# Optimization experiments

Hardware: AMD Instinct MI355X
Metric: run time of the kernel (lower is better)

Reference implementation:

```python
import jax, jax.numpy as jnp
import numpy as np

BN_EPS = 1e-3


def _bn(x, gamma, beta):
    # training-mode BatchNorm1d: per-call batch statistics (biased variance)
    m = jnp.mean(x, axis=0)
    v = jnp.mean(jnp.square(x - m), axis=0)
    return gamma * (x - m) * jax.lax.rsqrt(v + BN_EPS) + beta


def setup_inputs() -> dict:
    key = jax.random.key(0)
    ks = jax.random.split(key, 8)
    N, V, Cin, Cout = 1_000_000, 100_000, 16, 64
    return {
        "feat": jax.random.normal(ks[0], (V, Cin), dtype=jnp.float32),
        "points_xyz": jax.random.normal(ks[1], (N, Cin), dtype=jnp.float32),
        "unq_inv": jax.random.randint(ks[2], (N,), 0, V),
        "W_pre": jax.random.normal(ks[3], (Cin, Cout), dtype=jnp.float32) * (1.0 / np.sqrt(Cin)),
        "b_pre": jnp.zeros((Cout,), dtype=jnp.float32),
        "gamma_pre": jnp.ones((Cout,), dtype=jnp.float32),
        "beta_pre": jnp.zeros((Cout,), dtype=jnp.float32),
        "W_pos": jax.random.normal(ks[4], (Cout, Cout), dtype=jnp.float32) * (1.0 / np.sqrt(Cout)),
        "b_pos": jnp.zeros((Cout,), dtype=jnp.float32),
        "gamma_n": jnp.ones((Cout,), dtype=jnp.float32),
        "beta_n": jnp.zeros((Cout,), dtype=jnp.float32),
    }


def reference(feat, points_xyz, unq_inv, W_pre, b_pre, gamma_pre, beta_pre,
              W_pos, b_pos, gamma_n, beta_n):
    V = feat.shape[0]
    # per-point branch: pre_mix (Linear + BN), sin/cos gating, scatter-add to voxels
    p = _bn(points_xyz @ W_pre + b_pre, gamma_pre, beta_pre)      # [N, Cout]
    pw = p @ W_pos + b_pos                                        # [N, Cout]
    feat_add_sin = jax.ops.segment_sum(p * jnp.sin(pw), unq_inv, num_segments=V)  # [V, Cout]
    feat_add_cos = jax.ops.segment_sum(p * jnp.cos(pw), unq_inv, num_segments=V)
    # per-voxel (center) branch through the SAME pre_mix / pos_weight layers
    f = _bn(feat @ W_pre + b_pre, gamma_pre, beta_pre)            # [V, Cout]
    mw = f @ W_pos + b_pos
    center_sin = f * jnp.sin(mw)
    center_cos = f * jnp.cos(mw)
    final = (feat_add_sin + center_sin) * center_sin + (feat_add_cos + center_cos) * center_cos
    return jax.nn.relu(_bn(final, gamma_n, beta_n))
```

## Files before the change

kernel.cpp:

```cpp
#include <hip/hip_runtime.h>
#include <cstdint>
#include <cstddef>

constexpr int CIN  = 16;
constexpr int COUT = 64;
constexpr int NMOM = 16 + 136;
constexpr double BN_EPS = 1e-3;

typedef float v2f __attribute__((ext_vector_type(2)));
constexpr float INV_2PI = 0.15915494309189535f;

constexpr int P_A = 0, P_B = 64, P_C = 128, P_WC = 192, P_SZ = 192 + CIN * COUT;

constexpr int CHUNK = 512;
constexpr int MB = 256;

__global__ __launch_bounds__(256) void moments2_kernel(const float* __restrict__ xyz, int n1,
                                                       const float* __restrict__ feat, int n2,
                                                       const int* __restrict__ unq,
                                                       int* __restrict__ cnt,
                                                       float* __restrict__ partP,
                                                       float* __restrict__ partF)
{
    const int bb  = blockIdx.x;
    const bool second = (bb >= MB);
    const float* x = second ? feat : xyz;
    const int    n = second ? n2 : n1;
    float* part    = second ? partF : partP;
    const int blk  = second ? bb - MB : bb;

    float acc[NMOM];
#pragma unroll
    for (int i = 0; i < NMOM; i++) acc[i] = 0.f;

    int tid = blk * 256 + threadIdx.x;
    int stride = MB * 256;
    for (int r = tid; r < n; r += stride) {
        const float4* xp = (const float4*)(x + (size_t)r * CIN);
        float4 a0 = xp[0], a1 = xp[1], a2 = xp[2], a3 = xp[3];
        if (!second) atomicAdd(cnt + unq[r], 1);
        float v[16] = {a0.x,a0.y,a0.z,a0.w, a1.x,a1.y,a1.z,a1.w,
                       a2.x,a2.y,a2.z,a2.w, a3.x,a3.y,a3.z,a3.w};
#pragma unroll
        for (int i = 0; i < 16; i++) acc[i] += v[i];
        int c = 16;
#pragma unroll
        for (int k = 0; k < 16; k++)
#pragma unroll
            for (int l = k; l < 16; l++) { acc[c] = fmaf(v[k], v[l], acc[c]); c++; }
    }

    const int lane = threadIdx.x & 63;
    const int wid  = threadIdx.x >> 6;
    float r0 = 0.f, r1 = 0.f, r2 = 0.f;
#pragma unroll
    for (int i = 0; i < NMOM; i++) {
        float s = acc[i];
#pragma unroll
        for (int off = 1; off < 64; off <<= 1) s += __shfl_xor(s, off, 64);
        if (i < 64)       { if (lane == i)       r0 = s; }
        else if (i < 128) { if (lane == i - 64)  r1 = s; }
        else              { if (lane == i - 128) r2 = s; }
    }

    __shared__ float red[4][NMOM];
    red[wid][lane] = r0;
    red[wid][64 + lane] = r1;
    if (lane < NMOM - 128) red[wid][128 + lane] = r2;
    __syncthreads();
    int t = threadIdx.x;
    if (t < NMOM) {
        float s = red[0][t] + red[1][t] + red[2][t] + red[3][t];
        part[(size_t)blk * NMOM + t] = s;
    }
}

__global__ __launch_bounds__(256) void prep_kernel(const float* __restrict__ Wpre, const float* __restrict__ bpre,
                            const float* __restrict__ gpre, const float* __restrict__ bepre,
                            const float* __restrict__ Wpos, const float* __restrict__ bpos,
                            const float* __restrict__ partP, const float* __restrict__ partF,
                            int nrows, int Np, int Vv,
                            float* __restrict__ prepP, float* __restrict__ prepF)
{
    const int t  = threadIdx.x;
    const int br = blockIdx.x;
    const float* part = br ? partF : partP;
    const double n    = br ? (double)Vv : (double)Np;
    const double inv_n = 1.0 / n;
    float* prep       = br ? prepF : prepP;

    __shared__ float sWpre[CIN * 64];
    __shared__ float sWpos[64 * 64];
    __shared__ double mom[NMOM];
    __shared__ double sS[64], sB[64];

    for (int i = t; i < CIN * 64; i += 256) sWpre[i] = Wpre[i];
    for (int i = t; i < 64 * 64; i += 256)  sWpos[i] = Wpos[i];

    if (t < NMOM) {
        double s0 = 0, s1 = 0, s2 = 0, s3 = 0, s4 = 0, s5 = 0, s6 = 0, s7 = 0;
        int r = 0;
        for (; r + 8 <= nrows; r += 8) {
            s0 += (double)part[(size_t)(r + 0) * NMOM + t];
            s1 += (double)part[(size_t)(r + 1) * NMOM + t];
            s2 += (double)part[(size_t)(r + 2) * NMOM + t];
            s3 += (double)part[(size_t)(r + 3) * NMOM + t];
            s4 += (double)part[(size_t)(r + 4) * NMOM + t];
            s5 += (double)part[(size_t)(r + 5) * NMOM + t];
            s6 += (double)part[(size_t)(r + 6) * NMOM + t];
            s7 += (double)part[(size_t)(r + 7) * NMOM + t];
        }
        for (; r < nrows; r++) s0 += (double)part[(size_t)r * NMOM + t];
        mom[t] = ((s0 + s1) + (s2 + s3)) + ((s4 + s5) + (s6 + s7));
    }
    __syncthreads();

    if (t < 64) {
        const int k = t;
        double mu[16];
#pragma unroll
        for (int i = 0; i < 16; i++) mu[i] = mom[i] * inv_n;
        double w[16];
#pragma unroll
        for (int i = 0; i < 16; i++) w[i] = (double)sWpre[i * 64 + k];

        double mk = (double)bpre[k];
#pragma unroll
        for (int i = 0; i < 16; i++) mk += mu[i] * w[i];

        double var = 0.0;
        int c = 16;
#pragma unroll
        for (int a = 0; a < 16; a++)
#pragma unroll
            for (int l = a; l < 16; l++) {
                double cov = mom[c] * inv_n - mu[a] * mu[l]; c++;
                var += (a == l ? 1.0 : 2.0) * w[a] * w[l] * cov;
            }

        double s_k = (double)gpre[k] / sqrt(var + BN_EPS);
        double B_k = (double)bepre[k] + s_k * ((double)bpre[k] - mk);
        sS[k] = s_k; sB[k] = B_k;
    }
    __syncthreads();

    if (t < 64) {
        const int k = t;
        double c0 = (double)bpos[k], c1 = 0.0;
        for (int j = 0; j < 64; j += 2) {
            c0 += sB[j]     * (double)sWpos[j * 64 + k];
            c1 += sB[j + 1] * (double)sWpos[(j + 1) * 64 + k];
        }
        prep[P_A + k] = (float)sS[k];
        prep[P_B + k] = (float)sB[k];
        prep[P_C + k] = (float)(c0 + c1);
    }

    {
        const int k  = t & 63;
        const int i0 = t >> 6;
        for (int i = i0; i < 16; i += 4) {
            double w0 = 0.0, w1 = 0.0;
            for (int j = 0; j < 64; j += 2) {
                w0 += (double)sWpre[i * 64 + j]     * sS[j]     * (double)sWpos[j * 64 + k];
                w1 += (double)sWpre[i * 64 + j + 1] * sS[j + 1] * (double)sWpos[(j + 1) * 64 + k];
            }
            prep[P_WC + i * 64 + k] = (float)(w0 + w1);
        }
    }
}

__global__ __launch_bounds__(256) void scan_a(const int* __restrict__ cnt, int V,
                                              int* __restrict__ chunkSum)
{
    const int b = blockIdx.x, t = threadIdx.x;
    int base = b * CHUNK;
    int i0 = base + t * 2, i1 = i0 + 1;
    int s = ((i0 < V) ? cnt[i0] : 0) + ((i1 < V) ? cnt[i1] : 0);
    __shared__ int red[4];
    const int lane = t & 63, wid = t >> 6;
#pragma unroll
    for (int off = 1; off < 64; off <<= 1) s += __shfl_xor(s, off, 64);
    if (lane == 0) red[wid] = s;
    __syncthreads();
    if (t == 0) chunkSum[b] = red[0] + red[1] + red[2] + red[3];
}

__global__ __launch_bounds__(256) void scan_b(const int* __restrict__ chunkSum, int nch,
                                              int* __restrict__ chunkBase,
                                              int* __restrict__ start, int V, int N)
{
    const int t = threadIdx.x;
    __shared__ int a[256];
    int v = (t < nch) ? chunkSum[t] : 0;
    a[t] = v;
    __syncthreads();
    for (int off = 1; off < 256; off <<= 1) {
        int add = (t >= off) ? a[t - off] : 0;
        __syncthreads();
        a[t] += add;
        __syncthreads();
    }
    chunkBase[t] = a[t] - v;
    if (t == 0) start[V] = N;
}

__global__ __launch_bounds__(64) void scan_c(const int* __restrict__ cnt, int V,
                                             const int* __restrict__ chunkBase,
                                             int* __restrict__ start)
{
    const int b = blockIdx.x;
    const int lane = threadIdx.x;
    const int base = b * CHUNK + lane * 8;
    int e[8];
    int run = 0;
#pragma unroll
    for (int j = 0; j < 8; j++) {
        int idx = base + j;
        int c = (idx < V) ? cnt[idx] : 0;
        e[j] = run;
        run += c;
    }
    int incl = run;
#pragma unroll
    for (int off = 1; off < 64; off <<= 1) {
        int vv = __shfl_up(incl, off, 64);
        if (lane >= off) incl += vv;
    }
    int excl = incl - run;
    int myBase = chunkBase[b] + excl;
#pragma unroll
    for (int j = 0; j < 8; j++) {
        int idx = base + j;
        if (idx < V) start[idx] = myBase + e[j];
    }
}

__global__ __launch_bounds__(256) void scatter_kernel(const int* __restrict__ unq, int N,
                                                      const int* __restrict__ start,
                                                      int* __restrict__ cursor,
                                                      int* __restrict__ sortedIdx)
{
    int t = blockIdx.x * blockDim.x + threadIdx.x;
    int stride = gridDim.x * blockDim.x;
    for (; t < N; t += stride) {
        int v = unq[t];
        int pos = start[v] + atomicAdd(cursor + v, 1);
        sortedIdx[pos] = t;
    }
}

__global__ __launch_bounds__(256) void fused_pass(const float* __restrict__ xyz,
                                                  const float* __restrict__ feat,
                                                  const int* __restrict__ sortedIdx,
                                                  const int* __restrict__ start,
                                                  const float* __restrict__ Wpre,
                                                  const float* __restrict__ prepP,
                                                  const float* __restrict__ prepF,
                                                  float* __restrict__ outFinal,
                                                  float* __restrict__ statsPart, int V)
{
    const int lane = threadIdx.x & 63;
    const int wid  = threadIdx.x >> 6;
    const int rq   = lane >> 2;
    const int cc   = lane & 3;

    __shared__ float4 ldsq[4][3][64];
    __shared__ float  sWcF[CIN * 64];
    float4* bufA = ldsq[wid][0];
    float4* bufB = ldsq[wid][1];
    float4* remb = ldsq[wid][2];
    const int wslot = rq * 4 + cc;

    for (int i = threadIdx.x; i < CIN * 64; i += 256) sWcF[i] = prepF[P_WC + i];
    __syncthreads();

    v2f wP[16];
#pragma unroll
    for (int i = 0; i < 16; i++)
        wP[i] = (v2f){Wpre[i * 64 + lane], prepP[P_WC + i * 64 + lane]};

    const float AP = prepP[P_A + lane], BP = prepP[P_B + lane];
    const float CPr = prepP[P_C + lane] * INV_2PI;
    const float AF = prepF[P_A + lane], BF = prepF[P_B + lane];
    const float CFr = prepF[P_C + lane] * INV_2PI;

    const int wave = __builtin_amdgcn_readfirstlane((int)((blockIdx.x * blockDim.x + threadIdx.x) >> 6));
    const int nw   = (gridDim.x * blockDim.x) >> 6;
    float s1 = 0.f, s2 = 0.f;

    auto prefetch = [&](int v, int& sb, int& m, float4& q) {
        sb = __builtin_amdgcn_readfirstlane(start[v]);
        int se = __builtin_amdgcn_readfirstlane(start[v + 1]);
        m = se - sb;
        int ms0 = min(m, 15);
        int row = min(rq, ms0);
        int ridx = sortedIdx[sb + row];
        const float* bp = (row == ms0) ? (feat + (size_t)v * CIN)
                                       : (xyz  + (size_t)ridx * CIN);
        q = *(const float4*)(bp + cc * 4);
    };

    auto pointrow = [&](const float4* buf, int j, v2f& acc) {
        float4 c0 = buf[j * 4 + 0], c1 = buf[j * 4 + 1],
               c2 = buf[j * 4 + 2], c3 = buf[j * 4 + 3];
        float xs[16] = {c0.x,c0.y,c0.z,c0.w, c1.x,c1.y,c1.z,c1.w,
                        c2.x,c2.y,c2.z,c2.w, c3.x,c3.y,c3.z,c3.w};
        v2f d = (v2f){0.f, 0.f};
#pragma unroll
        for (int i = 0; i < 16; i++) d += xs[i] * wP[i];
        float p  = fmaf(AP, d.x, BP);
        float r  = fmaf(d.y, INV_2PI, CPr);
        float sv = __builtin_amdgcn_sinf(r);
        float cv = __builtin_amdgcn_cosf(r);
        acc += p * (v2f){sv, cv};
    };

    int v = wave;
    int sb = 0, m = 0;
    float4* cur = bufA;
    float4* nxt = bufB;
    if (v < V) {
        float4 q; prefetch(v, sb, m, q);
        cur[wslot] = q;
    }

    while (v < V) {
        const int vn = v + nw;
        int sbn = 0, mn = 0; float4 qn = {};
        if (vn < V) prefetch(vn, sbn, mn, qn);

        const int ms0 = min(m, 15);
        v2f acc = (v2f){0.f, 0.f};

        for (int j = 0; j < ms0; j++) pointrow(cur, j, acc);

        for (int base = 15; base < m; base += 16) {
            const int msr  = min(16, m - base);
            const int rowc = min(rq, msr - 1);
            int ridx = sortedIdx[sb + base + rowc];
            remb[wslot] = *(const float4*)(xyz + (size_t)ridx * CIN + cc * 4);
            for (int j = 0; j < msr; j++) pointrow(remb, j, acc);
        }

        {
            float4 c0 = cur[ms0 * 4 + 0], c1 = cur[ms0 * 4 + 1],
                   c2 = cur[ms0 * 4 + 2], c3 = cur[ms0 * 4 + 3];
            float xs[16] = {c0.x,c0.y,c0.z,c0.w, c1.x,c1.y,c1.z,c1.w,
                            c2.x,c2.y,c2.z,c2.w, c3.x,c3.y,c3.z,c3.w};
            float dx = 0.f, dw = 0.f;
#pragma unroll
            for (int i = 0; i < 16; i++) {
                dx = fmaf(xs[i], wP[i].x, dx);
                dw = fmaf(xs[i], sWcF[i * 64 + lane], dw);
            }
            float f  = fmaf(AF, dx, BF);
            float r  = fmaf(dw, INV_2PI, CFr);
            float sv = __builtin_amdgcn_sinf(r);
            float cv = __builtin_amdgcn_cosf(r);
            float cs = f * sv, ccn = f * cv;
            float fin = fmaf(acc.x + cs, cs, (acc.y + ccn) * ccn);
            outFinal[(size_t)v * 64 + lane] = fin;
            s1 += fin;
            s2 = fmaf(fin, fin, s2);
        }

        if (vn < V) nxt[wslot] = qn;
        float4* tmp = cur; cur = nxt; nxt = tmp;
        v = vn; sb = sbn; m = mn;
    }

    __shared__ float sh1[4][64], sh2[4][64];
    sh1[wid][lane] = s1; sh2[wid][lane] = s2;
    __syncthreads();
    if (threadIdx.x < 64) {
        float t1 = sh1[0][lane] + sh1[1][lane] + sh1[2][lane] + sh1[3][lane];
        float t2 = sh2[0][lane] + sh2[1][lane] + sh2[2][lane] + sh2[3][lane];
        float* row = statsPart + (size_t)(blockIdx.x & 63) * 128;
        atomicAdd(row + lane, t1);
        atomicAdd(row + 64 + lane, t2);
    }
}

__global__ __launch_bounds__(256) void norm_kernel(float* __restrict__ out,
                                                   const float* __restrict__ sp,
                                                   const float* __restrict__ gn,
                                                   const float* __restrict__ bnb,
                                                   int V, size_t n4)
{
    __shared__ float sNs[64], sNb[64];
    const int t = threadIdx.x;
    if (t < 64) {
        double u1 = 0.0, u2 = 0.0;
#pragma unroll 4
        for (int r = 0; r < 64; r++) {
            u1 += (double)sp[(size_t)r * 128 + t];
            u2 += (double)sp[(size_t)r * 128 + 64 + t];
        }
        double mean = u1 / (double)V;
        double var  = u2 / (double)V - mean * mean;
        double ns   = (double)gn[t] / sqrt(var + BN_EPS);
        sNs[t] = (float)ns;
        sNb[t] = (float)((double)bnb[t] - ns * mean);
    }
    __syncthreads();

    const float4* ns4 = (const float4*)sNs;
    const float4* nb4 = (const float4*)sNb;
    float4* o4 = (float4*)out;
    size_t i = (size_t)blockIdx.x * blockDim.x + threadIdx.x;
    size_t stride = (size_t)gridDim.x * blockDim.x;
    for (; i < n4; i += stride) {
        int g = (int)(i & 15);
        float4 sc = ns4[g], bi = nb4[g];
        float4 w = o4[i];
        w.x = fmaxf(0.f, fmaf(sc.x, w.x, bi.x));
        w.y = fmaxf(0.f, fmaf(sc.y, w.y, bi.y));
        w.z = fmaxf(0.f, fmaf(sc.z, w.z, bi.z));
        w.w = fmaxf(0.f, fmaf(sc.w, w.w, bi.w));
        o4[i] = w;
    }
}

extern "C" void kernel_launch(void* const* d_in, const int* in_sizes, int n_in,
                              void* d_out, int out_size, void* d_ws, size_t ws_size,
                              hipStream_t stream)
{
    const float* feat  = (const float*)d_in[0];
    const float* xyz   = (const float*)d_in[1];
    const int*   unq   = (const int*)d_in[2];
    const float* Wpre  = (const float*)d_in[3];
    const float* bpre  = (const float*)d_in[4];
    const float* gpre  = (const float*)d_in[5];
    const float* bepre = (const float*)d_in[6];
    const float* Wpos  = (const float*)d_in[7];
    const float* bpos  = (const float*)d_in[8];
    const float* gn    = (const float*)d_in[9];
    const float* bnb   = (const float*)d_in[10];

    const int V = in_sizes[0] / CIN;
    const int N = in_sizes[1] / CIN;
    const int nch = (V + CHUNK - 1) / CHUNK;

    char* ws = (char*)d_ws;
    size_t off = 0;
    auto alloc = [&](size_t bytes) { void* p = ws + off; off += (bytes + 255) & ~size_t(255); return p; };

    int*   cnt       = (int*)alloc((size_t)V * 4);
    int*   cursor    = (int*)alloc((size_t)V * 4);
    float* statsPart = (float*)alloc(64 * 128 * 4);
    const size_t zeroBytes = off;

    int*   start     = (int*)alloc((size_t)(V + 1) * 4);
    int*   chunkSum  = (int*)alloc(256 * 4);
    int*   chunkBase = (int*)alloc(256 * 4);
    int*   sortedIdx = (int*)alloc((size_t)(N + 64) * 4);

    float* partP = (float*)alloc((size_t)MB * NMOM * 4);
    float* partF = (float*)alloc((size_t)MB * NMOM * 4);
    float* prepP = (float*)alloc(P_SZ * 4);
    float* prepF = (float*)alloc(P_SZ * 4);

    hipMemsetAsync(d_ws, 0, zeroBytes, stream);

    moments2_kernel<<<2 * MB, 256, 0, stream>>>(xyz, N, feat, V, unq, cnt, partP, partF);
    scan_a<<<nch, 256, 0, stream>>>(cnt, V, chunkSum);
    scan_b<<<1, 256, 0, stream>>>(chunkSum, nch, chunkBase, start, V, N);
    scan_c<<<nch, 64, 0, stream>>>(cnt, V, chunkBase, start);
    scatter_kernel<<<1024, 256, 0, stream>>>(unq, N, start, cursor, sortedIdx);
    prep_kernel<<<2, 256, 0, stream>>>(Wpre, bpre, gpre, bepre, Wpos, bpos,
                                       partP, partF, MB, N, V, prepP, prepF);
    fused_pass<<<2048, 256, 0, stream>>>(xyz, feat, sortedIdx, start, Wpre,
                                         prepP, prepF, (float*)d_out, statsPart, V);
    norm_kernel<<<512, 256, 0, stream>>>((float*)d_out, statsPart, gn, bnb, V,
                                         (size_t)out_size / 4);
}
```

Measured before the change: 233.8 us.

## Merge prep with scan chunk sums, fold scan_b into scanC, software-pipeline LDS row loads

```diff
diff --git a/kernel.cpp b/kernel.cpp
--- a/kernel.cpp
+++ b/kernel.cpp
@@ -75,14 +75,32 @@
     }
 }
 
-__global__ __launch_bounds__(256) void prep_kernel(const float* __restrict__ Wpre, const float* __restrict__ bpre,
+__global__ __launch_bounds__(256) void prep_scanA(const float* __restrict__ Wpre, const float* __restrict__ bpre,
                             const float* __restrict__ gpre, const float* __restrict__ bepre,
                             const float* __restrict__ Wpos, const float* __restrict__ bpos,
                             const float* __restrict__ partP, const float* __restrict__ partF,
                             int nrows, int Np, int Vv,
-                            float* __restrict__ prepP, float* __restrict__ prepF)
-{
-    const int t  = threadIdx.x;
+                            float* __restrict__ prepP, float* __restrict__ prepF,
+                            const int* __restrict__ cnt, int V,
+                            int* __restrict__ chunkSum)
+{
+    const int t = threadIdx.x;
+    const int lane = t & 63, wid = t >> 6;
+
+    if (blockIdx.x >= 2) {
+        const int b = blockIdx.x - 2;
+        int base = b * CHUNK;
+        int i0 = base + t * 2, i1 = i0 + 1;
+        int s = ((i0 < V) ? cnt[i0] : 0) + ((i1 < V) ? cnt[i1] : 0);
+        __shared__ int redc[4];
+#pragma unroll
+        for (int off = 1; off < 64; off <<= 1) s += __shfl_xor(s, off, 64);
+        if (lane == 0) redc[wid] = s;
+        __syncthreads();
+        if (t == 0) chunkSum[b] = redc[0] + redc[1] + redc[2] + redc[3];
+        return;
+    }
+
     const int br = blockIdx.x;
     const float* part = br ? partF : partP;
     const double n    = br ? (double)Vv : (double)Np;
@@ -170,47 +188,20 @@
     }
 }
 
-__global__ __launch_bounds__(256) void scan_a(const int* __restrict__ cnt, int V,
-                                              int* __restrict__ chunkSum)
-{
-    const int b = blockIdx.x, t = threadIdx.x;
-    int base = b * CHUNK;
-    int i0 = base + t * 2, i1 = i0 + 1;
-    int s = ((i0 < V) ? cnt[i0] : 0) + ((i1 < V) ? cnt[i1] : 0);
-    __shared__ int red[4];
-    const int lane = t & 63, wid = t >> 6;
-#pragma unroll
-    for (int off = 1; off < 64; off <<= 1) s += __shfl_xor(s, off, 64);
-    if (lane == 0) red[wid] = s;
-    __syncthreads();
-    if (t == 0) chunkSum[b] = red[0] + red[1] + red[2] + red[3];
-}
-
-__global__ __launch_bounds__(256) void scan_b(const int* __restrict__ chunkSum, int nch,
-                                              int* __restrict__ chunkBase,
-                                              int* __restrict__ start, int V, int N)
-{
-    const int t = threadIdx.x;
-    __shared__ int a[256];
-    int v = (t < nch) ? chunkSum[t] : 0;
-    a[t] = v;
-    __syncthreads();
-    for (int off = 1; off < 256; off <<= 1) {
-        int add = (t >= off) ? a[t - off] : 0;
-        __syncthreads();
-        a[t] += add;
-        __syncthreads();
-    }
-    chunkBase[t] = a[t] - v;
-    if (t == 0) start[V] = N;
-}
-
-__global__ __launch_bounds__(64) void scan_c(const int* __restrict__ cnt, int V,
-                                             const int* __restrict__ chunkBase,
-                                             int* __restrict__ start)
+__global__ __launch_bounds__(64) void scanC(const int* __restrict__ cnt, int V, int N,
+                                            const int* __restrict__ chunkSum,
+                                            int* __restrict__ start,
+                                            int* __restrict__ cursor)
 {
     const int b = blockIdx.x;
     const int lane = threadIdx.x;
+
+    int pv = 0;
+    for (int i = lane; i < b; i += 64) pv += chunkSum[i];
+#pragma unroll
+    for (int off = 1; off < 64; off <<= 1) pv += __shfl_xor(pv, off, 64);
+    const int chunkBase = pv;
+
     const int base = b * CHUNK + lane * 8;
     int e[8];
     int run = 0;
@@ -228,12 +219,13 @@
         if (lane >= off) incl += vv;
     }
     int excl = incl - run;
-    int myBase = chunkBase[b] + excl;
+    int myBase = chunkBase + excl;
 #pragma unroll
     for (int j = 0; j < 8; j++) {
         int idx = base + j;
-        if (idx < V) start[idx] = myBase + e[j];
-    }
+        if (idx < V) { start[idx] = myBase + e[j]; cursor[idx] = 0; }
+    }
+    if (b == 0 && lane == 0) start[V] = N;
 }
 
 __global__ __launch_bounds__(256) void scatter_kernel(const int* __restrict__ unq, int N,
@@ -301,9 +293,7 @@
         q = *(const float4*)(bp + cc * 4);
     };
 
-    auto pointrow = [&](const float4* buf, int j, v2f& acc) {
-        float4 c0 = buf[j * 4 + 0], c1 = buf[j * 4 + 1],
-               c2 = buf[j * 4 + 2], c3 = buf[j * 4 + 3];
+    auto pointmath = [&](float4 c0, float4 c1, float4 c2, float4 c3, v2f& acc) {
         float xs[16] = {c0.x,c0.y,c0.z,c0.w, c1.x,c1.y,c1.z,c1.w,
                         c2.x,c2.y,c2.z,c2.w, c3.x,c3.y,c3.z,c3.w};
         v2f d = (v2f){0.f, 0.f};
@@ -333,14 +323,24 @@
         const int ms0 = min(m, 15);
         v2f acc = (v2f){0.f, 0.f};
 
-        for (int j = 0; j < ms0; j++) pointrow(cur, j, acc);
+        if (ms0 > 0) {
+            float4 r0 = cur[0], r1 = cur[1], r2 = cur[2], r3 = cur[3];
+            for (int j = 0; j + 1 < ms0; j++) {
+                float4 n0 = cur[(j+1)*4+0], n1 = cur[(j+1)*4+1],
+                       n2 = cur[(j+1)*4+2], n3 = cur[(j+1)*4+3];
+                pointmath(r0, r1, r2, r3, acc);
+                r0 = n0; r1 = n1; r2 = n2; r3 = n3;
+            }
+            pointmath(r0, r1, r2, r3, acc);
+        }
 
         for (int base = 15; base < m; base += 16) {
             const int msr  = min(16, m - base);
             const int rowc = min(rq, msr - 1);
             int ridx = sortedIdx[sb + base + rowc];
             remb[wslot] = *(const float4*)(xyz + (size_t)ridx * CIN + cc * 4);
-            for (int j = 0; j < msr; j++) pointrow(remb, j, acc);
+            for (int j = 0; j < msr; j++)
+                pointmath(remb[j*4+0], remb[j*4+1], remb[j*4+2], remb[j*4+3], acc);
         }
 
         {
@@ -447,13 +447,12 @@
     auto alloc = [&](size_t bytes) { void* p = ws + off; off += (bytes + 255) & ~size_t(255); return p; };
 
     int*   cnt       = (int*)alloc((size_t)V * 4);
-    int*   cursor    = (int*)alloc((size_t)V * 4);
     float* statsPart = (float*)alloc(64 * 128 * 4);
     const size_t zeroBytes = off;
 
+    int*   cursor    = (int*)alloc((size_t)V * 4);
     int*   start     = (int*)alloc((size_t)(V + 1) * 4);
     int*   chunkSum  = (int*)alloc(256 * 4);
-    int*   chunkBase = (int*)alloc(256 * 4);
     int*   sortedIdx = (int*)alloc((size_t)(N + 64) * 4);
 
     float* partP = (float*)alloc((size_t)MB * NMOM * 4);
@@ -464,12 +463,11 @@
     hipMemsetAsync(d_ws, 0, zeroBytes, stream);
 
     moments2_kernel<<<2 * MB, 256, 0, stream>>>(xyz, N, feat, V, unq, cnt, partP, partF);
-    scan_a<<<nch, 256, 0, stream>>>(cnt, V, chunkSum);
-    scan_b<<<1, 256, 0, stream>>>(chunkSum, nch, chunkBase, start, V, N);
-    scan_c<<<nch, 64, 0, stream>>>(cnt, V, chunkBase, start);
+    prep_scanA<<<nch + 2, 256, 0, stream>>>(Wpre, bpre, gpre, bepre, Wpos, bpos,
+                                            partP, partF, MB, N, V, prepP, prepF,
+                                            cnt, V, chunkSum);
+    scanC<<<nch, 64, 0, stream>>>(cnt, V, N, chunkSum, start, cursor);
     scatter_kernel<<<1024, 256, 0, stream>>>(unq, N, start, cursor, sortedIdx);
-    prep_kernel<<<2, 256, 0, stream>>>(Wpre, bpre, gpre, bepre, Wpos, bpos,
-                                       partP, partF, MB, N, V, prepP, prepF);
     fused_pass<<<2048, 256, 0, stream>>>(xyz, feat, sortedIdx, start, Wpre,
                                          prepP, prepF, (float*)d_out, statsPart, V);
     norm_kernel<<<512, 256, 0, stream>>>((float*)d_out, statsPart, gn, bnb, V,
```

After: 244.8 us. 1.05x slower.

## Add per-voxel 16-slot index table and deepen prefetch pipeline to two voxels

Applied to the files above, without the earlier changes.

```diff
diff --git a/kernel.cpp b/kernel.cpp
--- a/kernel.cpp
+++ b/kernel.cpp
@@ -239,37 +239,41 @@
 __global__ __launch_bounds__(256) void scatter_kernel(const int* __restrict__ unq, int N,
                                                       const int* __restrict__ start,
                                                       int* __restrict__ cursor,
-                                                      int* __restrict__ sortedIdx)
+                                                      int* __restrict__ sortedIdx,
+                                                      int* __restrict__ table16)
 {
     int t = blockIdx.x * blockDim.x + threadIdx.x;
     int stride = gridDim.x * blockDim.x;
     for (; t < N; t += stride) {
         int v = unq[t];
-        int pos = start[v] + atomicAdd(cursor + v, 1);
-        sortedIdx[pos] = t;
+        int slot = atomicAdd(cursor + v, 1);
+        sortedIdx[start[v] + slot] = t;
+        if (slot < 15) table16[v * 16 + slot] = t;
     }
 }
 
 __global__ __launch_bounds__(256) void fused_pass(const float* __restrict__ xyz,
                                                   const float* __restrict__ feat,
+                                                  const int* __restrict__ table16,
+                                                  const int* __restrict__ cnt,
                                                   const int* __restrict__ sortedIdx,
                                                   const int* __restrict__ start,
                                                   const float* __restrict__ Wpre,
                                                   const float* __restrict__ prepP,
                                                   const float* __restrict__ prepF,
                                                   float* __restrict__ outFinal,
-                                                  float* __restrict__ statsPart, int V)
+                                                  float* __restrict__ statsPart,
+                                                  int V, int N)
 {
     const int lane = threadIdx.x & 63;
     const int wid  = threadIdx.x >> 6;
     const int rq   = lane >> 2;
     const int cc   = lane & 3;
 
-    __shared__ float4 ldsq[4][3][64];
+    __shared__ float4 ldsq[4][2][64];
     __shared__ float  sWcF[CIN * 64];
-    float4* bufA = ldsq[wid][0];
-    float4* bufB = ldsq[wid][1];
-    float4* remb = ldsq[wid][2];
+    float4* cur = ldsq[wid][0];
+    float4* nxt = ldsq[wid][1];
     const int wslot = rq * 4 + cc;
 
     for (int i = threadIdx.x; i < CIN * 64; i += 256) sWcF[i] = prepF[P_WC + i];
@@ -289,19 +293,20 @@
     const int nw   = (gridDim.x * blockDim.x) >> 6;
     float s1 = 0.f, s2 = 0.f;
 
-    auto prefetch = [&](int v, int& sb, int& m, float4& q) {
-        sb = __builtin_amdgcn_readfirstlane(start[v]);
-        int se = __builtin_amdgcn_readfirstlane(start[v + 1]);
-        m = se - sb;
-        int ms0 = min(m, 15);
-        int row = min(rq, ms0);
-        int ridx = sortedIdx[sb + row];
-        const float* bp = (row == ms0) ? (feat + (size_t)v * CIN)
-                                       : (xyz  + (size_t)ridx * CIN);
+    auto issueIdx = [&](int v, int& cReg, int& tReg) {
+        cReg = cnt[v];
+        tReg = table16[v * 16 + rq];
+    };
+    auto gatherRow = [&](int v, int tIdx, float4& q) {
+        const float* bp;
+        if (rq == 15) bp = feat + (size_t)v * CIN;
+        else {
+            int ridx = min(max(tIdx, 0), N - 1);
+            bp = xyz + (size_t)ridx * CIN;
+        }
         q = *(const float4*)(bp + cc * 4);
     };
-
-    auto pointrow = [&](const float4* buf, int j, v2f& acc) {
+    auto pointmath = [&](const float4* buf, int j, v2f& acc) {
         float4 c0 = buf[j * 4 + 0], c1 = buf[j * 4 + 1],
                c2 = buf[j * 4 + 2], c3 = buf[j * 4 + 3];
         float xs[16] = {c0.x,c0.y,c0.z,c0.w, c1.x,c1.y,c1.z,c1.w,
@@ -316,36 +321,44 @@
         acc += p * (v2f){sv, cv};
     };
 
-    int v = wave;
-    int sb = 0, m = 0;
-    float4* cur = bufA;
-    float4* nxt = bufB;
-    if (v < V) {
-        float4 q; prefetch(v, sb, m, q);
+    int v0 = wave, v1 = v0 + nw, v2 = v1 + nw;
+    int m0 = 0, m1 = 0, c2r = 0, t2r = 0;
+    float4 q1 = {};
+
+    if (v0 < V) {
+        int c, t; issueIdx(v0, c, t);
+        m0 = __builtin_amdgcn_readfirstlane(c);
+        float4 q; gatherRow(v0, t, q);
         cur[wslot] = q;
     }
-
-    while (v < V) {
-        const int vn = v + nw;
-        int sbn = 0, mn = 0; float4 qn = {};
-        if (vn < V) prefetch(vn, sbn, mn, qn);
-
-        const int ms0 = min(m, 15);
+    if (v1 < V) {
+        int c, t; issueIdx(v1, c, t);
+        m1 = __builtin_amdgcn_readfirstlane(c);
+        gatherRow(v1, t, q1);
+    }
+    if (v2 < V) issueIdx(v2, c2r, t2r);
+
+    while (v0 < V) {
+        const int ms0 = min(m0, 15);
         v2f acc = (v2f){0.f, 0.f};
 
-        for (int j = 0; j < ms0; j++) pointrow(cur, j, acc);
-
-        for (int base = 15; base < m; base += 16) {
-            const int msr  = min(16, m - base);
-            const int rowc = min(rq, msr - 1);
-            int ridx = sortedIdx[sb + base + rowc];
-            remb[wslot] = *(const float4*)(xyz + (size_t)ridx * CIN + cc * 4);
-            for (int j = 0; j < msr; j++) pointrow(remb, j, acc);
+        for (int j = 0; j < ms0; j++) pointmath(cur, j, acc);
+
+        if (m0 > 15) {
+            const int sb = __builtin_amdgcn_readfirstlane(start[v0]);
+            for (int base = 15; base < m0; base += 16) {
+                const int msr  = min(16, m0 - base);
+                const int rowc = min(rq, msr - 1);
+                int ridx = sortedIdx[sb + base + rowc];
+                nxt[wslot] = *(const float4*)(xyz + (size_t)ridx * CIN + cc * 4);
+                for (int j = 0; j < msr; j++)
+                    pointmath(nxt, j, acc);
+            }
         }
 
         {
-            float4 c0 = cur[ms0 * 4 + 0], c1 = cur[ms0 * 4 + 1],
-                   c2 = cur[ms0 * 4 + 2], c3 = cur[ms0 * 4 + 3];
+            float4 c0 = cur[15 * 4 + 0], c1 = cur[15 * 4 + 1],
+                   c2 = cur[15 * 4 + 2], c3 = cur[15 * 4 + 3];
             float xs[16] = {c0.x,c0.y,c0.z,c0.w, c1.x,c1.y,c1.z,c1.w,
                             c2.x,c2.y,c2.z,c2.w, c3.x,c3.y,c3.z,c3.w};
             float dx = 0.f, dw = 0.f;
@@ -360,14 +373,23 @@
             float cv = __builtin_amdgcn_cosf(r);
             float cs = f * sv, ccn = f * cv;
             float fin = fmaf(acc.x + cs, cs, (acc.y + ccn) * ccn);
-            outFinal[(size_t)v * 64 + lane] = fin;
+            outFinal[(size_t)v0 * 64 + lane] = fin;
             s1 += fin;
             s2 = fmaf(fin, fin, s2);
         }
 
-        if (vn < V) nxt[wslot] = qn;
+        if (v1 < V) nxt[wslot] = q1;
+        int mNew = 0; float4 qNew = {};
+        if (v2 < V) {
+            mNew = __builtin_amdgcn_readfirstlane(c2r);
+            gatherRow(v2, t2r, qNew);
+        }
+        const int v3 = v2 + nw;
+        if (v3 < V) issueIdx(v3, c2r, t2r);
+
         float4* tmp = cur; cur = nxt; nxt = tmp;
-        v = vn; sb = sbn; m = mn;
+        v0 = v1; v1 = v2; v2 = v3;
+        m0 = m1; m1 = mNew; q1 = qNew;
     }
 
     __shared__ float sh1[4][64], sh2[4][64];
@@ -455,6 +477,7 @@
     int*   chunkSum  = (int*)alloc(256 * 4);
     int*   chunkBase = (int*)alloc(256 * 4);
     int*   sortedIdx = (int*)alloc((size_t)(N + 64) * 4);
+    int*   table16   = (int*)alloc((size_t)V * 16 * 4);
 
     float* partP = (float*)alloc((size_t)MB * NMOM * 4);
     float* partF = (float*)alloc((size_t)MB * NMOM * 4);
@@ -467,11 +490,11 @@
     scan_a<<<nch, 256, 0, stream>>>(cnt, V, chunkSum);
     scan_b<<<1, 256, 0, stream>>>(chunkSum, nch, chunkBase, start, V, N);
     scan_c<<<nch, 64, 0, stream>>>(cnt, V, chunkBase, start);
-    scatter_kernel<<<1024, 256, 0, stream>>>(unq, N, start, cursor, sortedIdx);
+    scatter_kernel<<<1024, 256, 0, stream>>>(unq, N, start, cursor, sortedIdx, table16);
     prep_kernel<<<2, 256, 0, stream>>>(Wpre, bpre, gpre, bepre, Wpos, bpos,
                                        partP, partF, MB, N, V, prepP, prepF);
-    fused_pass<<<2048, 256, 0, stream>>>(xyz, feat, sortedIdx, start, Wpre,
-                                         prepP, prepF, (float*)d_out, statsPart, V);
+    fused_pass<<<2048, 256, 0, stream>>>(xyz, feat, table16, cnt, sortedIdx, start,
+                                         Wpre, prepP, prepF, (float*)d_out, statsPart, V, N);
     norm_kernel<<<512, 256, 0, stream>>>((float*)d_out, statsPart, gn, bnb, V,
                                          (size_t)out_size / 4);
 }
```

Measured after the change: 257.0 us. 1.1x slower.

## Use packed fp16 dot products for per-point projections in fused pass

Applied to the files above, without the earlier changes.

```diff
diff --git a/kernel.cpp b/kernel.cpp
--- a/kernel.cpp
+++ b/kernel.cpp
@@ -8,12 +8,16 @@
 constexpr double BN_EPS = 1e-3;
 
 typedef float v2f __attribute__((ext_vector_type(2)));
+typedef __fp16 v2h __attribute__((ext_vector_type(2)));
 constexpr float INV_2PI = 0.15915494309189535f;
 
 constexpr int P_A = 0, P_B = 64, P_C = 128, P_WC = 192, P_SZ = 192 + CIN * COUT;
 
 constexpr int CHUNK = 512;
-constexpr int MB = 256;
+constexpr int MB = 512;
+
+__device__ __forceinline__ unsigned bc_u(v2h h) { return __builtin_bit_cast(unsigned, h); }
+__device__ __forceinline__ v2h bc_h(unsigned u) { return __builtin_bit_cast(v2h, u); }
 
 __global__ __launch_bounds__(256) void moments2_kernel(const float* __restrict__ xyz, int n1,
                                                        const float* __restrict__ feat, int n2,
@@ -265,20 +269,28 @@
     const int rq   = lane >> 2;
     const int cc   = lane & 3;
 
-    __shared__ float4 ldsq[4][3][64];
-    __shared__ float  sWcF[CIN * 64];
-    float4* bufA = ldsq[wid][0];
-    float4* bufB = ldsq[wid][1];
-    float4* remb = ldsq[wid][2];
+    __shared__ uint2 ldsq[4][3][64];
+    __shared__ unsigned sWcF2[8 * 64];
+    uint2* bufA = ldsq[wid][0];
+    uint2* bufB = ldsq[wid][1];
+    uint2* remb = ldsq[wid][2];
     const int wslot = rq * 4 + cc;
 
-    for (int i = threadIdx.x; i < CIN * 64; i += 256) sWcF[i] = prepF[P_WC + i];
-    __syncthreads();
-
-    v2f wP[16];
-#pragma unroll
-    for (int i = 0; i < 16; i++)
-        wP[i] = (v2f){Wpre[i * 64 + lane], prepP[P_WC + i * 64 + lane]};
+    for (int i = threadIdx.x; i < 8 * 64; i += 256) {
+        int fi = i >> 6, ch = i & 63;
+        sWcF2[i] = bc_u(__builtin_amdgcn_cvt_pkrtz(prepF[P_WC + (2 * fi) * 64 + ch],
+                                                   prepF[P_WC + (2 * fi + 1) * 64 + ch]));
+    }
+    __syncthreads();
+
+    v2h wpre2[8], wcp2[8];
+#pragma unroll
+    for (int i = 0; i < 8; i++) {
+        wpre2[i] = __builtin_amdgcn_cvt_pkrtz(Wpre[(2 * i) * 64 + lane],
+                                              Wpre[(2 * i + 1) * 64 + lane]);
+        wcp2[i]  = __builtin_amdgcn_cvt_pkrtz(prepP[P_WC + (2 * i) * 64 + lane],
+                                              prepP[P_WC + (2 * i + 1) * 64 + lane]);
+    }
 
     const float AP = prepP[P_A + lane], BP = prepP[P_B + lane];
     const float CPr = prepP[P_C + lane] * INV_2PI;
@@ -289,7 +301,7 @@
     const int nw   = (gridDim.x * blockDim.x) >> 6;
     float s1 = 0.f, s2 = 0.f;
 
-    auto prefetch = [&](int v, int& sb, int& m, float4& q) {
+    auto prefetch = [&](int v, int& sb, int& m, uint2& u) {
         sb = __builtin_amdgcn_readfirstlane(start[v]);
         int se = __builtin_amdgcn_readfirstlane(start[v + 1]);
         m = se - sb;
@@ -298,19 +310,24 @@
         int ridx = sortedIdx[sb + row];
         const float* bp = (row == ms0) ? (feat + (size_t)v * CIN)
                                        : (xyz  + (size_t)ridx * CIN);
-        q = *(const float4*)(bp + cc * 4);
+        float4 q = *(const float4*)(bp + cc * 4);
+        u.x = bc_u(__builtin_amdgcn_cvt_pkrtz(q.x, q.y));
+        u.y = bc_u(__builtin_amdgcn_cvt_pkrtz(q.z, q.w));
     };
 
-    auto pointrow = [&](const float4* buf, int j, v2f& acc) {
-        float4 c0 = buf[j * 4 + 0], c1 = buf[j * 4 + 1],
-               c2 = buf[j * 4 + 2], c3 = buf[j * 4 + 3];
-        float xs[16] = {c0.x,c0.y,c0.z,c0.w, c1.x,c1.y,c1.z,c1.w,
-                        c2.x,c2.y,c2.z,c2.w, c3.x,c3.y,c3.z,c3.w};
-        v2f d = (v2f){0.f, 0.f};
-#pragma unroll
-        for (int i = 0; i < 16; i++) d += xs[i] * wP[i];
-        float p  = fmaf(AP, d.x, BP);
-        float r  = fmaf(d.y, INV_2PI, CPr);
+    auto pointmath = [&](const uint2* buf, int j, v2f& acc) {
+        uint4 a = ((const uint4*)buf)[j * 2 + 0];
+        uint4 b = ((const uint4*)buf)[j * 2 + 1];
+        v2h xs[8] = {bc_h(a.x), bc_h(a.y), bc_h(a.z), bc_h(a.w),
+                     bc_h(b.x), bc_h(b.y), bc_h(b.z), bc_h(b.w)};
+        float dx = 0.f, dw = 0.f;
+#pragma unroll
+        for (int i = 0; i < 8; i++) {
+            dx = __builtin_amdgcn_fdot2(xs[i], wpre2[i], dx, false);
+            dw = __builtin_amdgcn_fdot2(xs[i], wcp2[i],  dw, false);
+        }
+        float p  = fmaf(AP, dx, BP);
+        float r  = fmaf(dw, INV_2PI, CPr);
         float sv = __builtin_amdgcn_sinf(r);
         float cv = __builtin_amdgcn_cosf(r);
         acc += p * (v2f){sv, cv};
@@ -318,41 +335,45 @@
 
     int v = wave;
     int sb = 0, m = 0;
-    float4* cur = bufA;
-    float4* nxt = bufB;
+    uint2* cur = bufA;
+    uint2* nxt = bufB;
     if (v < V) {
-        float4 q; prefetch(v, sb, m, q);
-        cur[wslot] = q;
+        uint2 u; prefetch(v, sb, m, u);
+        cur[wslot] = u;
     }
 
     while (v < V) {
         const int vn = v + nw;
-        int sbn = 0, mn = 0; float4 qn = {};
-        if (vn < V) prefetch(vn, sbn, mn, qn);
+        int sbn = 0, mn = 0; uint2 un = {};
+        if (vn < V) prefetch(vn, sbn, mn, un);
 
         const int ms0 = min(m, 15);
         v2f acc = (v2f){0.f, 0.f};
 
-        for (int j = 0; j < ms0; j++) pointrow(cur, j, acc);
+        for (int j = 0; j < ms0; j++) pointmath(cur, j, acc);
 
         for (int base = 15; base < m; base += 16) {
             const int msr  = min(16, m - base);
             const int rowc = min(rq, msr - 1);
             int ridx = sortedIdx[sb + base + rowc];
-            remb[wslot] = *(const float4*)(xyz + (size_t)ridx * CIN + cc * 4);
-            for (int j = 0; j < msr; j++) pointrow(remb, j, acc);
+            float4 q = *(const float4*)(xyz + (size_t)ridx * CIN + cc * 4);
+            uint2 u;
+            u.x = bc_u(__builtin_amdgcn_cvt_pkrtz(q.x, q.y));
+            u.y = bc_u(__builtin_amdgcn_cvt_pkrtz(q.z, q.w));
+            remb[wslot] = u;
+            for (int j = 0; j < msr; j++) pointmath(remb, j, acc);
         }
 
         {
-            float4 c0 = cur[ms0 * 4 + 0], c1 = cur[ms0 * 4 + 1],
-                   c2 = cur[ms0 * 4 + 2], c3 = cur[ms0 * 4 + 3];
-            float xs[16] = {c0.x,c0.y,c0.z,c0.w, c1.x,c1.y,c1.z,c1.w,
-                            c2.x,c2.y,c2.z,c2.w, c3.x,c3.y,c3.z,c3.w};
+            uint4 a = ((const uint4*)cur)[ms0 * 2 + 0];
+            uint4 b = ((const uint4*)cur)[ms0 * 2 + 1];
+            v2h xs[8] = {bc_h(a.x), bc_h(a.y), bc_h(a.z), bc_h(a.w),
+                         bc_h(b.x), bc_h(b.y), bc_h(b.z), bc_h(b.w)};
             float dx = 0.f, dw = 0.f;
 #pragma unroll
-            for (int i = 0; i < 16; i++) {
-                dx = fmaf(xs[i], wP[i].x, dx);
-                dw = fmaf(xs[i], sWcF[i * 64 + lane], dw);
+            for (int i = 0; i < 8; i++) {
+                dx = __builtin_amdgcn_fdot2(xs[i], wpre2[i], dx, false);
+                dw = __builtin_amdgcn_fdot2(xs[i], bc_h(sWcF2[i * 64 + lane]), dw, false);
             }
             float f  = fmaf(AF, dx, BF);
             float r  = fmaf(dw, INV_2PI, CFr);
@@ -365,8 +386,8 @@
             s2 = fmaf(fin, fin, s2);
         }
 
-        if (vn < V) nxt[wslot] = qn;
-        float4* tmp = cur; cur = nxt; nxt = tmp;
+        if (vn < V) nxt[wslot] = un;
+        uint2* tmp = cur; cur = nxt; nxt = tmp;
         v = vn; sb = sbn; m = mn;
     }
 
```

New measurement: 260.5 us. 1.11x slower.
